# Kernel tuning notes

Hardware: AMD Instinct MI355X
Metric: run time of the kernel (lower is better)

## Reference

```python
import jax, jax.numpy as jnp
import numpy as np

DIM = 1024
N_HEADS = 16
HEAD_DIM = DIM // N_HEADS


def setup_inputs() -> dict:
    key = jax.random.key(0)
    k_x, k_qkv_w, k_qkv_b, k_p_w, k_p_b = jax.random.split(key, 5)
    s = 1.0 / np.sqrt(DIM)
    return {
        "x": jax.random.normal(k_x, (2, 2048, DIM), dtype=jnp.float32),
        # stored as [in, out] so forward is x @ W + b (equivalent to torch Linear)
        "qkv_w": jax.random.uniform(k_qkv_w, (DIM, 3 * DIM), minval=-s, maxval=s, dtype=jnp.float32),
        "qkv_b": jax.random.uniform(k_qkv_b, (3 * DIM,), minval=-s, maxval=s, dtype=jnp.float32),
        "proj_w": jax.random.uniform(k_p_w, (DIM, DIM), minval=-s, maxval=s, dtype=jnp.float32),
        "proj_b": jax.random.uniform(k_p_b, (DIM,), minval=-s, maxval=s, dtype=jnp.float32),
    }


def reference(x, qkv_w, qkv_b, proj_w, proj_b):
    b, s, _ = x.shape
    qkv = x @ qkv_w + qkv_b                       # [b, s, 3*dim]
    q, k, v = jnp.split(qkv, 3, axis=-1)
    def split_heads(t):
        return t.reshape(b, s, N_HEADS, HEAD_DIM).transpose(0, 2, 1, 3)  # [b, h, s, d]
    q, k, v = map(split_heads, (q, k, v))
    scale = 1.0 / np.sqrt(HEAD_DIM)
    scores = jnp.einsum("bhqd,bhkd->bhqk", q, k) * scale
    attn = jax.nn.softmax(scores, axis=-1)
    out = jnp.einsum("bhqk,bhkd->bhqd", attn, v)
    out = out.transpose(0, 2, 1, 3).reshape(b, s, DIM)
    return out @ proj_w + proj_b
```

## Files before the change

kernel.cpp:

```cpp
#include <hip/hip_runtime.h>
#include <hip/hip_bf16.h>

typedef __attribute__((ext_vector_type(8))) short bf16x8;
typedef __attribute__((ext_vector_type(4))) float f32x4;
typedef __attribute__((ext_vector_type(16))) float f32x16;
typedef __attribute__((ext_vector_type(4))) unsigned short u16x4;
typedef __attribute__((ext_vector_type(8))) unsigned short u16x8v;

#define S_LEN 2048
#define NHEAD 16
#define HDIM 64
#define DIM 1024

__device__ __forceinline__ unsigned short f2bf(float f) {
    union { float f; unsigned u; } x; x.f = f;
    unsigned r = x.u + 0x7FFFu + ((x.u >> 16) & 1u);
    return (unsigned short)(r >> 16);
}
__device__ __forceinline__ unsigned short f2bf_fast(float f) {
    union { float f; unsigned u; } x; x.f = f;
    return (unsigned short)((x.u + 0x8000u) >> 16);
}

__device__ __forceinline__ f32x4 mfma16(bf16x8 a, bf16x8 b, f32x4 c) {
    return __builtin_amdgcn_mfma_f32_16x16x32_bf16(a, b, c, 0, 0, 0);
}
__device__ __forceinline__ f32x16 mfma32(bf16x8 a, bf16x8 b, f32x16 c) {
    return __builtin_amdgcn_mfma_f32_32x32x16_bf16(a, b, c, 0, 0, 0);
}

__device__ __forceinline__ float fexp2(float x) {
#if __has_builtin(__builtin_amdgcn_exp2f)
    return __builtin_amdgcn_exp2f(x);
#else
    return exp2f(x);
#endif
}

__device__ __forceinline__ void gl_lds16(const void* g, void* l) {
    __builtin_amdgcn_global_load_lds(
        (const __attribute__((address_space(1))) unsigned int*)g,
        (__attribute__((address_space(3))) unsigned int*)l, 16, 0, 0);
}

__global__ __launch_bounds__(256) void xconv_kernel(const float* __restrict__ X,
                                                    unsigned short* __restrict__ Xb) {
    size_t i = ((size_t)blockIdx.x * 256 + threadIdx.x) * 8;
    float4 a = *reinterpret_cast<const float4*>(&X[i]);
    float4 b = *reinterpret_cast<const float4*>(&X[i + 4]);
    u16x8v o;
    o[0] = f2bf(a.x); o[1] = f2bf(a.y); o[2] = f2bf(a.z); o[3] = f2bf(a.w);
    o[4] = f2bf(b.x); o[5] = f2bf(b.y); o[6] = f2bf(b.z); o[7] = f2bf(b.w);
    *reinterpret_cast<u16x8v*>(&Xb[i]) = o;
}

__global__ __launch_bounds__(256) void wtrans_kernel(const float* __restrict__ W,
                                                     unsigned short* __restrict__ Wt,
                                                     int K, int N) {
    __shared__ float lds[64][65];
    int k0 = blockIdx.x * 64, n0 = blockIdx.y * 64;
    int tid = threadIdx.x;
    for (int idx = tid; idx < 1024; idx += 256) {
        int row = idx >> 4, c = (idx & 15) << 2;
        float4 v = *reinterpret_cast<const float4*>(&W[(size_t)(k0 + row) * N + n0 + c]);
        lds[row][c] = v.x; lds[row][c + 1] = v.y; lds[row][c + 2] = v.z; lds[row][c + 3] = v.w;
    }
    __syncthreads();
    for (int idx = tid; idx < 1024; idx += 256) {
        int row = idx >> 4, c = (idx & 15) << 2;
        u16x4 o;
        o[0] = f2bf(lds[c][row]);     o[1] = f2bf(lds[c + 1][row]);
        o[2] = f2bf(lds[c + 2][row]); o[3] = f2bf(lds[c + 3][row]);
        *reinterpret_cast<u16x4*>(&Wt[(size_t)(n0 + row) * K + k0 + c]) = o;
    }
}

template <int MODE>
__global__ __launch_bounds__(256) void gemm_kernel(
    const unsigned short* __restrict__ Ab, const unsigned short* __restrict__ Bt,
    const float* __restrict__ bias,
    unsigned short* __restrict__ Qb, unsigned short* __restrict__ Kb,
    unsigned short* __restrict__ Vt, float* __restrict__ outf) {
    __shared__ unsigned short Alds[128 * 64];
    __shared__ unsigned short Blds[128 * 64];
    const int tid = threadIdx.x;
    const int m0 = blockIdx.x * 128, n0 = blockIdx.y * 128;
    const int wid = tid >> 6, lane = tid & 63;
    const int wm = wid >> 1, wn = wid & 1;
    const int lr = lane & 15, lg = lane >> 4;

    const char* Abase = (const char*)(Ab + (size_t)m0 * 1024);
    const char* Bbase = (const char*)(Bt + (size_t)n0 * 1024);

    int srcOff[4], dstOff[4];
#pragma unroll
    for (int i = 0; i < 4; ++i) {
        int off = i * 4096 + wid * 1024 + lane * 16;
        int row = off >> 7, col = off & 127;
        srcOff[i] = row * 2048 + (col ^ ((row & 7) << 4));
        dstOff[i] = off;
    }
    const int swz = (lr & 7) << 4;

    f32x4 acc[4][4] = {};

    for (int kt = 0; kt < 16; ++kt) {
        __syncthreads();
#pragma unroll
        for (int i = 0; i < 4; ++i) {
            gl_lds16(Abase + srcOff[i] + kt * 128, (char*)Alds + dstOff[i]);
            gl_lds16(Bbase + srcOff[i] + kt * 128, (char*)Blds + dstOff[i]);
        }
        __syncthreads();

#pragma unroll
        for (int ks = 0; ks < 2; ++ks) {
            bf16x8 af[4], bfr[4];
#pragma unroll
            for (int i = 0; i < 4; ++i)
                af[i] = *reinterpret_cast<const bf16x8*>(
                    (const char*)Alds + (wm * 64 + i * 16 + lr) * 128 + ((ks * 64 + lg * 16) ^ swz));
#pragma unroll
            for (int j = 0; j < 4; ++j)
                bfr[j] = *reinterpret_cast<const bf16x8*>(
                    (const char*)Blds + (wn * 64 + j * 16 + lr) * 128 + ((ks * 64 + lg * 16) ^ swz));
            __builtin_amdgcn_s_setprio(1);
#pragma unroll
            for (int i = 0; i < 4; ++i)
#pragma unroll
                for (int j = 0; j < 4; ++j)
                    acc[i][j] = mfma16(af[i], bfr[j], acc[i][j]);
            __builtin_amdgcn_s_setprio(0);
        }
    }

    if constexpr (MODE == 0) {
        const int sec = n0 >> 10;
#pragma unroll
        for (int j = 0; j < 4; ++j) {
            int gn = n0 + wn * 64 + j * 16 + lr;
            float bv = bias[gn];
            int nn = gn & 1023, h = nn >> 6, d = nn & 63;
#pragma unroll
            for (int i = 0; i < 4; ++i) {
#pragma unroll
                for (int r = 0; r < 4; ++r) {
                    int m = m0 + wm * 64 + i * 16 + lg * 4 + r;
                    int b_ = m >> 11, s_ = m & 2047;
                    size_t bh = (size_t)(b_ * NHEAD + h);
                    float v = acc[i][j][r] + bv;
                    if (sec == 0)
                        Qb[(bh * S_LEN + s_) * HDIM + d] = f2bf(v * 0.18033688f);
                    else if (sec == 1)
                        Kb[(bh * S_LEN + s_) * HDIM + d] = f2bf(v);
                    else
                        Vt[(bh * HDIM + d) * S_LEN + s_] = f2bf(v);
                }
            }
        }
    } else {
#pragma unroll
        for (int j = 0; j < 4; ++j) {
            int gn = n0 + wn * 64 + j * 16 + lr;
            float bv = bias[gn];
#pragma unroll
            for (int i = 0; i < 4; ++i) {
#pragma unroll
                for (int r = 0; r < 4; ++r) {
                    int m = m0 + wm * 64 + i * 16 + lg * 4 + r;
                    outf[(size_t)m * DIM + gn] = acc[i][j][r] + bv;
                }
            }
        }
    }
}

#define PST 72
#define NT (S_LEN / 64)
__global__ __launch_bounds__(256) void attn_kernel(const unsigned short* __restrict__ Qb,
                                                   const unsigned short* __restrict__ Kb,
                                                   const unsigned short* __restrict__ Vt,
                                                   unsigned short* __restrict__ Ob) {
    __shared__ unsigned short Klds[2][64 * 64];
    __shared__ unsigned short Vlds[2][64 * 64];
    __shared__ unsigned short Plds[4][32 * PST];
    const int bh = blockIdx.y;
    const int wid = threadIdx.x >> 6;
    const int lane = threadIdx.x & 63;
    const int l31 = lane & 31, hi = lane >> 5;
    const int q0 = blockIdx.x * 128 + wid * 32;
    unsigned short* pl = Plds[wid];

    const unsigned short* qrow = &Qb[((size_t)bh * S_LEN + q0 + l31) * HDIM];
    bf16x8 qf[4];
#pragma unroll
    for (int kst = 0; kst < 4; ++kst)
        qf[kst] = *reinterpret_cast<const bf16x8*>(&qrow[kst * 16 + hi * 8]);

    const char* kT = (const char*)&Kb[(size_t)bh * S_LEN * HDIM];
    const char* vT = (const char*)&Vt[(size_t)bh * HDIM * S_LEN];

    const int Lb0 = (wid * 2 + 0) * 1024 + lane * 16;
    const int Lb1 = (wid * 2 + 1) * 1024 + lane * 16;
    const int row0 = Lb0 >> 7, row1 = Lb1 >> 7;
    const int sw0 = (Lb0 & 127) ^ ((row0 & 7) << 4);
    const int sw1 = (Lb1 & 127) ^ ((row1 & 7) << 4);
    const int dst0 = wid * 2048, dst1 = wid * 2048 + 1024;

    float lsum[16];
#pragma unroll
    for (int r = 0; r < 16; ++r) lsum[r] = 0.f;
    f32x16 acc[2] = {};

    {
        char* kl = (char*)Klds[0]; char* vl = (char*)Vlds[0];
        gl_lds16(kT + row0 * 128 + sw0, kl + dst0);
        gl_lds16(kT + row1 * 128 + sw1, kl + dst1);
        gl_lds16(vT + row0 * 4096 + sw0, vl + dst0);
        gl_lds16(vT + row1 * 4096 + sw1, vl + dst1);
    }

    int cur = 0;
    for (int jt = 0; jt < NT; ++jt) {
        __syncthreads();
        if (jt + 1 < NT) {
            char* kl = (char*)Klds[cur ^ 1]; char* vl = (char*)Vlds[cur ^ 1];
            size_t kof = (size_t)(jt + 1) * 8192, vof = (size_t)(jt + 1) * 128;
            gl_lds16(kT + kof + row0 * 128 + sw0, kl + dst0);
            gl_lds16(kT + kof + row1 * 128 + sw1, kl + dst1);
            gl_lds16(vT + vof + row0 * 4096 + sw0, vl + dst0);
            gl_lds16(vT + vof + row1 * 4096 + sw1, vl + dst1);
        }
        const char* kl = (const char*)Klds[cur];
        const char* vl = (const char*)Vlds[cur];

        f32x16 p[2] = {};
        __builtin_amdgcn_s_setprio(1);
#pragma unroll
        for (int ct = 0; ct < 2; ++ct) {
            const int s = ct * 32 + l31;
            const char* krow = kl + s * 128;
            const int swz = ((s & 7) << 4);
#pragma unroll
            for (int kst = 0; kst < 4; ++kst) {
                bf16x8 kb = *reinterpret_cast<const bf16x8*>(krow + ((kst * 32 + hi * 16) ^ swz));
                p[ct] = mfma32(qf[kst], kb, p[ct]);
            }
        }
        __builtin_amdgcn_s_setprio(0);

#pragma unroll
        for (int ct = 0; ct < 2; ++ct)
#pragma unroll
            for (int r = 0; r < 16; ++r) {
                float e = fexp2(p[ct][r]);
                lsum[r] += e;
                int rq = (r & 3) + 8 * (r >> 2) + 4 * hi;
                pl[rq * PST + ct * 32 + l31] = f2bf_fast(e);
            }

        bf16x8 pa[4];
#pragma unroll
        for (int kst = 0; kst < 4; ++kst)
            pa[kst] = *reinterpret_cast<bf16x8*>(&pl[l31 * PST + kst * 16 + hi * 8]);
        __builtin_amdgcn_s_setprio(1);
#pragma unroll
        for (int dt = 0; dt < 2; ++dt) {
            const int d = dt * 32 + l31;
            const char* vrow = vl + d * 128;
            const int swz = ((d & 7) << 4);
#pragma unroll
            for (int kst = 0; kst < 4; ++kst) {
                bf16x8 vb = *reinterpret_cast<const bf16x8*>(vrow + ((kst * 32 + hi * 16) ^ swz));
                acc[dt] = mfma32(pa[kst], vb, acc[dt]);
            }
        }
        __builtin_amdgcn_s_setprio(0);

        __syncthreads();
        cur ^= 1;
    }

#pragma unroll
    for (int off = 1; off < 32; off <<= 1)
#pragma unroll
        for (int r = 0; r < 16; ++r) lsum[r] += __shfl_xor(lsum[r], off, 64);

    const int b_ = bh >> 4, h = bh & 15;
#pragma unroll
    for (int dt = 0; dt < 2; ++dt)
#pragma unroll
        for (int r = 0; r < 16; ++r) {
            int rq = (r & 3) + 8 * (r >> 2) + 4 * hi;
            float o = acc[dt][r] / lsum[r];
            int q = q0 + rq;
            Ob[((size_t)(b_ * S_LEN + q)) * DIM + h * HDIM + dt * 32 + l31] = f2bf_fast(o);
        }
}

extern "C" void kernel_launch(void* const* d_in, const int* in_sizes, int n_in,
                              void* d_out, int out_size, void* d_ws, size_t ws_size,
                              hipStream_t stream) {
    const float* x      = (const float*)d_in[0];
    const float* qkv_w  = (const float*)d_in[1];
    const float* qkv_b  = (const float*)d_in[2];
    const float* proj_w = (const float*)d_in[3];
    const float* proj_b = (const float*)d_in[4];
    float* out = (float*)d_out;

    unsigned short* Wqkvt = (unsigned short*)d_ws;
    unsigned short* Wpt   = Wqkvt + 3072 * 1024;
    unsigned short* Qb    = Wpt + 1024 * 1024;
    unsigned short* Kb    = Qb + 32 * 2048 * 64;
    unsigned short* Vt    = Kb + 32 * 2048 * 64;
    unsigned short* Ob    = Vt + 32 * 2048 * 64;
    unsigned short* Xb    = Ob + 4096 * 1024;

    xconv_kernel<<<2048, 256, 0, stream>>>(x, Xb);
    wtrans_kernel<<<dim3(16, 48), 256, 0, stream>>>(qkv_w, Wqkvt, 1024, 3072);
    wtrans_kernel<<<dim3(16, 16), 256, 0, stream>>>(proj_w, Wpt, 1024, 1024);

    gemm_kernel<0><<<dim3(32, 24), 256, 0, stream>>>(Xb, Wqkvt, qkv_b, Qb, Kb, Vt, nullptr);
    attn_kernel<<<dim3(16, 32), 256, 0, stream>>>(Qb, Kb, Vt, Ob);
    gemm_kernel<1><<<dim3(32, 8), 256, 0, stream>>>(Ob, Wpt, proj_b, nullptr, nullptr, nullptr, out);
}
```

Baseline: 127.0 us.

## Keep attention probabilities in registers via transposed QK^T and permlane swap

The QK^T MFMA now takes its operands in swapped order, so each lane holds scores for a single query row across keys. The probabilities are converted to bf16 with packed cvt and rearranged into the PV A-operand with v_permlane32_swap, which removes the shared-memory round trip for P. Row sums become one scalar per lane, reduced with one cross-half shuffle instead of a 16-register butterfly, and the final division becomes a reciprocal multiply. This relies on exact MFMA register layouts and on gfx950-specific instructions, and it also cuts LDS usage per block.

```diff
diff --git a/kernel.cpp b/kernel.cpp
--- a/kernel.cpp
+++ b/kernel.cpp
@@ -175,7 +175,6 @@
     }
 }
 
-#define PST 72
 #define NT (S_LEN / 64)
 __global__ __launch_bounds__(256) void attn_kernel(const unsigned short* __restrict__ Qb,
                                                    const unsigned short* __restrict__ Kb,
@@ -183,13 +182,11 @@
                                                    unsigned short* __restrict__ Ob) {
     __shared__ unsigned short Klds[2][64 * 64];
     __shared__ unsigned short Vlds[2][64 * 64];
-    __shared__ unsigned short Plds[4][32 * PST];
     const int bh = blockIdx.y;
     const int wid = threadIdx.x >> 6;
     const int lane = threadIdx.x & 63;
     const int l31 = lane & 31, hi = lane >> 5;
     const int q0 = blockIdx.x * 128 + wid * 32;
-    unsigned short* pl = Plds[wid];
 
     const unsigned short* qrow = &Qb[((size_t)bh * S_LEN + q0 + l31) * HDIM];
     bf16x8 qf[4];
@@ -207,9 +204,9 @@
     const int sw1 = (Lb1 & 127) ^ ((row1 & 7) << 4);
     const int dst0 = wid * 2048, dst1 = wid * 2048 + 1024;
 
-    float lsum[16];
-#pragma unroll
-    for (int r = 0; r < 16; ++r) lsum[r] = 0.f;
+    const int swz = (l31 & 7) << 4;
+
+    float ls = 0.f;
     f32x16 acc[2] = {};
 
     {
@@ -238,13 +235,11 @@
         __builtin_amdgcn_s_setprio(1);
 #pragma unroll
         for (int ct = 0; ct < 2; ++ct) {
-            const int s = ct * 32 + l31;
-            const char* krow = kl + s * 128;
-            const int swz = ((s & 7) << 4);
+            const char* krow = kl + (ct * 32 + l31) * 128;
 #pragma unroll
             for (int kst = 0; kst < 4; ++kst) {
                 bf16x8 kb = *reinterpret_cast<const bf16x8*>(krow + ((kst * 32 + hi * 16) ^ swz));
-                p[ct] = mfma32(qf[kst], kb, p[ct]);
+                p[ct] = mfma32(kb, qf[kst], p[ct]);
             }
         }
         __builtin_amdgcn_s_setprio(0);
@@ -254,21 +249,34 @@
 #pragma unroll
             for (int r = 0; r < 16; ++r) {
                 float e = fexp2(p[ct][r]);
-                lsum[r] += e;
-                int rq = (r & 3) + 8 * (r >> 2) + 4 * hi;
-                pl[rq * PST + ct * 32 + l31] = f2bf_fast(e);
+                p[ct][r] = e;
+                ls += e;
             }
 
         bf16x8 pa[4];
 #pragma unroll
-        for (int kst = 0; kst < 4; ++kst)
-            pa[kst] = *reinterpret_cast<bf16x8*>(&pl[l31 * PST + kst * 16 + hi * 8]);
+        for (int kst = 0; kst < 4; ++kst) {
+            const int ctq = kst >> 1, rb = 8 * (kst & 1);
+            unsigned aw[2], bw[2];
+#pragma unroll
+            for (int u = 0; u < 2; ++u) {
+                unsigned a, b;
+                asm("v_cvt_pk_bf16_f32 %0, %1, %2"
+                    : "=v"(a) : "v"(p[ctq][rb + 2 * u]), "v"(p[ctq][rb + 2 * u + 1]));
+                asm("v_cvt_pk_bf16_f32 %0, %1, %2"
+                    : "=v"(b) : "v"(p[ctq][rb + 4 + 2 * u]), "v"(p[ctq][rb + 4 + 2 * u + 1]));
+                asm volatile("v_permlane32_swap_b32 %0, %1" : "+v"(a), "+v"(b));
+                aw[u] = a; bw[u] = b;
+            }
+            union { unsigned w[4]; bf16x8 v; } pu;
+            pu.w[0] = aw[0]; pu.w[1] = aw[1]; pu.w[2] = bw[0]; pu.w[3] = bw[1];
+            pa[kst] = pu.v;
+        }
+
         __builtin_amdgcn_s_setprio(1);
 #pragma unroll
         for (int dt = 0; dt < 2; ++dt) {
-            const int d = dt * 32 + l31;
-            const char* vrow = vl + d * 128;
-            const int swz = ((d & 7) << 4);
+            const char* vrow = vl + (dt * 32 + l31) * 128;
 #pragma unroll
             for (int kst = 0; kst < 4; ++kst) {
                 bf16x8 vb = *reinterpret_cast<const bf16x8*>(vrow + ((kst * 32 + hi * 16) ^ swz));
@@ -281,10 +289,14 @@
         cur ^= 1;
     }
 
-#pragma unroll
-    for (int off = 1; off < 32; off <<= 1)
-#pragma unroll
-        for (int r = 0; r < 16; ++r) lsum[r] += __shfl_xor(lsum[r], off, 64);
+    ls += __shfl_xor(ls, 32, 64);
+
+    float inv[16];
+#pragma unroll
+    for (int r = 0; r < 16; ++r) {
+        int rq = (r & 3) + 8 * (r >> 2) + 4 * hi;
+        inv[r] = 1.f / __shfl(ls, rq, 64);
+    }
 
     const int b_ = bh >> 4, h = bh & 15;
 #pragma unroll
@@ -292,7 +304,7 @@
 #pragma unroll
         for (int r = 0; r < 16; ++r) {
             int rq = (r & 3) + 8 * (r >> 2) + 4 * hi;
-            float o = acc[dt][r] / lsum[r];
+            float o = acc[dt][r] * inv[r];
             int q = q0 + rq;
             Ob[((size_t)(b_ * S_LEN + q)) * DIM + h * HDIM + dt * 32 + l31] = f2bf_fast(o);
         }
```

Measured after the change: 120.7 us. 5.0% less time.
